# Performance work log

Hardware: AMD Instinct MI355X
Metric: run time of the kernel (lower is better)

Reference implementation:

```python
import jax, jax.numpy as jnp
import numpy as np

C_Z, H, C = 128, 4, 32
L = 320
SCALE = 1.0 / np.sqrt(C)
EPS = 1e-5


def setup_inputs() -> dict:
    key = jax.random.key(0)
    ks = jax.random.split(key, 8)
    s = 0.02
    return {
        "z": jax.random.normal(ks[0], (L, L, C_Z), dtype=jnp.float32),
        "pair_mask": jnp.ones((L, L), dtype=jnp.float32),
        "res_mask": jnp.ones((L,), dtype=bool),
        "ln_gamma": jnp.ones((C_Z,), dtype=jnp.float32),
        "ln_beta": jnp.zeros((C_Z,), dtype=jnp.float32),
        "Wq": jax.random.normal(ks[1], (C_Z, H * C), dtype=jnp.float32) * s,
        "Wk": jax.random.normal(ks[2], (C_Z, H * C), dtype=jnp.float32) * s,
        "Wv": jax.random.normal(ks[3], (C_Z, H * C), dtype=jnp.float32) * s,
        "Wb": jax.random.normal(ks[4], (C_Z, H), dtype=jnp.float32) * s,
        "Wg": jax.random.normal(ks[5], (C_Z, H * C), dtype=jnp.float32) * s,
        "Wout": jax.random.normal(ks[6], (H * C, C_Z), dtype=jnp.float32) * s,
    }


def _layernorm(x, gamma, beta):
    mu = jnp.mean(x, axis=-1, keepdims=True)
    var = jnp.mean(jnp.square(x - mu), axis=-1, keepdims=True)
    return (x - mu) * jax.lax.rsqrt(var + EPS) * gamma + beta


def reference(z, pair_mask, res_mask, ln_gamma, ln_beta, Wq, Wk, Wv, Wb, Wg, Wout):
    Ldim = z.shape[0]
    z_ln = _layernorm(z, ln_gamma, ln_beta)                      # [L,L,c_z]
    Q = (z_ln @ Wq).reshape(Ldim, Ldim, H, C)                    # [i,j,h,c]
    K = (z_ln @ Wk).reshape(Ldim, Ldim, H, C)                    # [i,k,h,c]
    V = (z_ln @ Wv).reshape(Ldim, Ldim, H, C)                    # [i,k,h,c]
    B = z_ln @ Wb                                                # [j,k,h]
    G = jax.nn.sigmoid(z_ln @ Wg).reshape(Ldim, Ldim, H, C)      # [i,j,h,c]

    # logits[i,h,j,k] = <Q[i,j], K[i,k]> * scale + B[j,k,h]
    logits = jnp.einsum("ijhc,ikhc->ihjk", Q, K) * SCALE
    logits = logits + jnp.transpose(B, (2, 0, 1))[None]          # +[1,h,j,k]
    neg_inf = jnp.asarray(-jnp.inf, logits.dtype)
    logits = jnp.where(res_mask[None, None, None, :], logits, neg_inf)
    attn = jax.nn.softmax(logits, axis=-1)                       # over k

    out = jnp.einsum("ihjk,ikhc->ijhc", attn, V)                 # [i,j,h,c]
    out = (G * out).reshape(Ldim, Ldim, H * C)
    dz = out @ Wout                                              # [L,L,c_z]
    return dz * pair_mask[..., None]
```

## Files before the change

### kernel.cpp

```cpp
#include <hip/hip_runtime.h>

#define LDIM 320
#define CZ 128
#define NH 4
#define CH 32
#define SCALE_QK 0.17677669529663687f
#define LN_EPS 1e-5f

typedef __attribute__((ext_vector_type(8))) short bf16x8;
typedef __attribute__((ext_vector_type(4))) float f32x4;

__device__ __forceinline__ unsigned int pack_bf2(float a, float b) {
  unsigned int ua = __float_as_uint(a);
  unsigned int ub = __float_as_uint(b);
  unsigned int ra = (ua + 0x7fffu + ((ua >> 16) & 1u)) >> 16;
  unsigned int rb = (ub + 0x7fffu + ((ub >> 16) & 1u)) >> 16;
  return (ra & 0xffffu) | (rb << 16);
}

__device__ __forceinline__ unsigned short f2bf(float a) {
  unsigned int ua = __float_as_uint(a);
  return (unsigned short)((ua + 0x7fffu + ((ua >> 16) & 1u)) >> 16);
}

__device__ __forceinline__ float bf2f(unsigned short u) {
  return __uint_as_float(((unsigned int)u) << 16);
}

__global__ __launch_bounds__(256) void k_prep(
    const float* __restrict__ Wq, const float* __restrict__ Wk,
    const float* __restrict__ Wv, const float* __restrict__ Wb,
    const float* __restrict__ Wg, const float* __restrict__ Wout,
    unsigned short* __restrict__ Wt, unsigned short* __restrict__ Woutt)
{
  __shared__ __attribute__((aligned(16))) unsigned short buf[64 * 136];
  const int t = threadIdx.x, bid = blockIdx.x;
  const bool isOut = (bid >= 9);
  const int n0 = isOut ? (bid - 9) * 64 : bid * 64;
  const int nl = t & 63;
  const int n = n0 + nl;
#pragma unroll 8
  for (int it = 0; it < 32; ++it) {
    const int k = (t >> 6) + 4 * it;
    float v;
    if (isOut)        v = Wout[k * 128 + n];
    else if (n < 128) v = Wq[k * 128 + n];
    else if (n < 256) v = Wk[k * 128 + n - 128];
    else if (n < 384) v = Wv[k * 128 + n - 256];
    else if (n < 512) v = Wg[k * 128 + n - 384];
    else if (n < 516) v = Wb[k * 4 + n - 512];
    else              v = 0.f;
    buf[nl * 136 + k] = f2bf(v);
  }
  __syncthreads();
  unsigned short* dst = isOut ? Woutt : Wt;
#pragma unroll
  for (int it = 0; it < 4; ++it) {
    const int idx = t + 256 * it;
    const int rr = idx >> 4, ck = idx & 15;
    const uint4 d = *(const uint4*)&buf[rr * 136 + ck * 8];
    *(uint4*)(dst + (size_t)(n0 + rr) * 128 + ck * 8) = d;
  }
}

__global__ __launch_bounds__(256) void k_lnproj(
    const float* __restrict__ z, const float* __restrict__ gamma,
    const float* __restrict__ beta, const unsigned short* __restrict__ Wt,
    unsigned short* __restrict__ Qg, unsigned short* __restrict__ Kg,
    unsigned short* __restrict__ Vg, unsigned short* __restrict__ Gg,
    float* __restrict__ Bh)
{
  __shared__ __attribute__((aligned(16))) unsigned short As[128 * 136];
  const int t = threadIdx.x;
  const int m0 = blockIdx.x * 128;
  const int rlane = t & 7;

  const float* gp = gamma + rlane * 16;
  const float* bp = beta + rlane * 16;
  const float4 g0 = *(const float4*)(gp + 0);
  const float4 g1 = *(const float4*)(gp + 4);
  const float4 g2 = *(const float4*)(gp + 8);
  const float4 g3 = *(const float4*)(gp + 12);
  const float4 b0 = *(const float4*)(bp + 0);
  const float4 b1 = *(const float4*)(bp + 4);
  const float4 b2 = *(const float4*)(bp + 8);
  const float4 b3 = *(const float4*)(bp + 12);

#pragma unroll
  for (int rr = 0; rr < 4; ++rr) {
    const int row = rr * 32 + (t >> 3);
    const float* zp = z + (size_t)(m0 + row) * CZ + rlane * 16;
    const float4 x0 = *(const float4*)(zp + 0);
    const float4 x1 = *(const float4*)(zp + 4);
    const float4 x2 = *(const float4*)(zp + 8);
    const float4 x3 = *(const float4*)(zp + 12);
    float s  = x0.x + x0.y + x0.z + x0.w + x1.x + x1.y + x1.z + x1.w +
               x2.x + x2.y + x2.z + x2.w + x3.x + x3.y + x3.z + x3.w;
    float ss = x0.x*x0.x + x0.y*x0.y + x0.z*x0.z + x0.w*x0.w +
               x1.x*x1.x + x1.y*x1.y + x1.z*x1.z + x1.w*x1.w +
               x2.x*x2.x + x2.y*x2.y + x2.z*x2.z + x2.w*x2.w +
               x3.x*x3.x + x3.y*x3.y + x3.z*x3.z + x3.w*x3.w;
    s  += __shfl_xor(s, 1);  ss += __shfl_xor(ss, 1);
    s  += __shfl_xor(s, 2);  ss += __shfl_xor(ss, 2);
    s  += __shfl_xor(s, 4);  ss += __shfl_xor(ss, 4);
    const float mu  = s * (1.f / 128.f);
    const float var = ss * (1.f / 128.f) - mu * mu;
    const float rs  = rsqrtf(var + LN_EPS);
    uint4 u0, u1;
    u0.x = pack_bf2((x0.x - mu) * rs * g0.x + b0.x, (x0.y - mu) * rs * g0.y + b0.y);
    u0.y = pack_bf2((x0.z - mu) * rs * g0.z + b0.z, (x0.w - mu) * rs * g0.w + b0.w);
    u0.z = pack_bf2((x1.x - mu) * rs * g1.x + b1.x, (x1.y - mu) * rs * g1.y + b1.y);
    u0.w = pack_bf2((x1.z - mu) * rs * g1.z + b1.z, (x1.w - mu) * rs * g1.w + b1.w);
    u1.x = pack_bf2((x2.x - mu) * rs * g2.x + b2.x, (x2.y - mu) * rs * g2.y + b2.y);
    u1.y = pack_bf2((x2.z - mu) * rs * g2.z + b2.z, (x2.w - mu) * rs * g2.w + b2.w);
    u1.z = pack_bf2((x3.x - mu) * rs * g3.x + b3.x, (x3.y - mu) * rs * g3.y + b3.y);
    u1.w = pack_bf2((x3.z - mu) * rs * g3.z + b3.z, (x3.w - mu) * rs * g3.w + b3.w);
    unsigned short* dst = &As[row * 136 + rlane * 16];
    *(uint4*)(dst + 0) = u0;
    *(uint4*)(dst + 8) = u1;
  }
  __syncthreads();

  const int w = t >> 6, lane = t & 63;
  const int m16 = lane & 15, qd = lane >> 4;
  const f32x4 z4 = {0.f, 0.f, 0.f, 0.f};

  bf16x8 af[2][4];
#pragma unroll
  for (int ks = 0; ks < 4; ++ks) {
    af[0][ks] = *(const bf16x8*)&As[(w * 32 + m16) * 136 + ks * 32 + qd * 8];
    af[1][ks] = *(const bf16x8*)&As[(w * 32 + 16 + m16) * 136 + ks * 32 + qd * 8];
  }

  for (int ntile = 0; ntile < 8; ++ntile) {
    f32x4 acc[2][4];
#pragma unroll
    for (int sub = 0; sub < 2; ++sub)
#pragma unroll
      for (int nt = 0; nt < 4; ++nt) acc[sub][nt] = z4;
#pragma unroll
    for (int ks = 0; ks < 4; ++ks) {
#pragma unroll
      for (int nt = 0; nt < 4; ++nt) {
        const bf16x8 bf = *(const bf16x8*)(
            Wt + (size_t)(ntile * 64 + nt * 16 + m16) * 128 + ks * 32 + qd * 8);
        acc[0][nt] = __builtin_amdgcn_mfma_f32_16x16x32_bf16(af[0][ks], bf, acc[0][nt], 0, 0, 0);
        acc[1][nt] = __builtin_amdgcn_mfma_f32_16x16x32_bf16(af[1][ks], bf, acc[1][nt], 0, 0, 0);
      }
    }
#pragma unroll
    for (int sub = 0; sub < 2; ++sub) {
#pragma unroll
      for (int r = 0; r < 4; ++r) {
        const int p = m0 + w * 32 + sub * 16 + qd * 4 + r;
        const int a = p / 320, bb = p - a * 320;
#pragma unroll
        for (int nt = 0; nt < 4; ++nt) {
          const int n = ntile * 64 + nt * 16 + m16;
          const int off = n & 127, hh = off >> 5, cc = off & 31;
          float val = acc[sub][nt][r];
          if (ntile >= 6) val = 1.f / (1.f + __expf(-val));
          unsigned short* dst =
              (ntile < 2 ? Qg : (ntile < 4 ? Kg : (ntile < 6 ? Vg : Gg)));
          dst[((size_t)(a * 4 + hh) * 320 + bb) * 32 + cc] = f2bf(val);
        }
      }
    }
  }

  {
    f32x4 acc0 = z4, acc1 = z4;
#pragma unroll
    for (int ks = 0; ks < 4; ++ks) {
      const bf16x8 bf = *(const bf16x8*)(
          Wt + (size_t)(512 + m16) * 128 + ks * 32 + qd * 8);
      acc0 = __builtin_amdgcn_mfma_f32_16x16x32_bf16(af[0][ks], bf, acc0, 0, 0, 0);
      acc1 = __builtin_amdgcn_mfma_f32_16x16x32_bf16(af[1][ks], bf, acc1, 0, 0, 0);
    }
    if (m16 < 4) {
#pragma unroll
      for (int r = 0; r < 4; ++r) {
        const int p0 = m0 + w * 32 + qd * 4 + r;
        Bh[(size_t)m16 * 102400 + p0] = acc0[r];
        Bh[(size_t)m16 * 102400 + p0 + 16] = acc1[r];
      }
    }
  }
}

__global__ __launch_bounds__(256) void k_attn(
    const unsigned short* __restrict__ Qg, const unsigned short* __restrict__ Kg,
    const unsigned short* __restrict__ Vg, const unsigned short* __restrict__ Gg,
    const float* __restrict__ Bh, const int* __restrict__ rmask,
    unsigned short* __restrict__ Obg)
{
  __shared__ __attribute__((aligned(16))) unsigned short Vt[32 * 328];
  __shared__ __attribute__((aligned(16))) unsigned short Ps[4][16 * 168];
  const int h = blockIdx.x, i = blockIdx.y;
  const int t = threadIdx.x;
  const size_t base = (size_t)(i * NH + h) * (LDIM * CH);

  {
    const int k0 = t >> 3, c4 = (t & 7) * 4;
#pragma unroll
    for (int it = 0; it < 10; ++it) {
      const int k = k0 + 32 * it;
      const uint2 d = *(const uint2*)(Vg + base + k * 32 + c4);
      Vt[(c4 + 0) * 328 + k] = (unsigned short)(d.x & 0xffffu);
      Vt[(c4 + 1) * 328 + k] = (unsigned short)(d.x >> 16);
      Vt[(c4 + 2) * 328 + k] = (unsigned short)(d.y & 0xffffu);
      Vt[(c4 + 3) * 328 + k] = (unsigned short)(d.y >> 16);
    }
  }
  __syncthreads();

  const int w = t >> 6, lane = t & 63;
  const int m16 = lane & 15, qd = lane >> 4;
  const f32x4 z4 = {0.f, 0.f, 0.f, 0.f};

  float mkr[20];
#pragma unroll
  for (int kt = 0; kt < 20; ++kt)
    mkr[kt] = rmask[kt * 16 + m16] ? 0.f : -INFINITY;

  for (int jt = w; jt < 20; jt += 4) {
    const bf16x8 qfrag =
        *(const bf16x8*)(Qg + base + (size_t)(jt * 16 + m16) * 32 + qd * 8);

    f32x4 acc[20];
#pragma unroll
    for (int kt = 0; kt < 20; ++kt) {
      const bf16x8 kf =
          *(const bf16x8*)(Kg + base + (size_t)(kt * 16 + m16) * 32 + qd * 8);
      acc[kt] = __builtin_amdgcn_mfma_f32_16x16x32_bf16(qfrag, kf, z4, 0, 0, 0);
    }

    const float* bp = Bh + (size_t)h * 102400 +
                      (size_t)(jt * 16 + qd * 4) * 320 + m16;
    float mx[4] = {-INFINITY, -INFINITY, -INFINITY, -INFINITY};
#pragma unroll
    for (int kt = 0; kt < 20; ++kt) {
#pragma unroll
      for (int r = 0; r < 4; ++r) {
        const float b = bp[r * 320 + kt * 16];
        const float s = fmaf(acc[kt][r], SCALE_QK, b) + mkr[kt];
        acc[kt][r] = s;
        mx[r] = fmaxf(mx[r], s);
      }
    }
#pragma unroll
    for (int r = 0; r < 4; ++r) {
      mx[r] = fmaxf(mx[r], __shfl_xor(mx[r], 1));
      mx[r] = fmaxf(mx[r], __shfl_xor(mx[r], 2));
      mx[r] = fmaxf(mx[r], __shfl_xor(mx[r], 4));
      mx[r] = fmaxf(mx[r], __shfl_xor(mx[r], 8));
    }
    float l[4] = {0.f, 0.f, 0.f, 0.f};
#pragma unroll
    for (int kt = 0; kt < 20; ++kt) {
#pragma unroll
      for (int r = 0; r < 4; ++r) {
        const float p = __expf(acc[kt][r] - mx[r]);
        acc[kt][r] = p;
        l[r] += p;
      }
    }
#pragma unroll
    for (int r = 0; r < 4; ++r) {
      l[r] += __shfl_xor(l[r], 1);
      l[r] += __shfl_xor(l[r], 2);
      l[r] += __shfl_xor(l[r], 4);
      l[r] += __shfl_xor(l[r], 8);
    }
    float rl[4];
#pragma unroll
    for (int r = 0; r < 4; ++r) rl[r] = 1.f / l[r];

    f32x4 accO0 = z4, accO1 = z4;
#pragma unroll
    for (int hh = 0; hh < 2; ++hh) {
      __syncthreads();
#pragma unroll
      for (int kt2 = 0; kt2 < 10; ++kt2) {
        const int kt = hh * 10 + kt2;
#pragma unroll
        for (int r = 0; r < 4; ++r)
          Ps[w][(qd * 4 + r) * 168 + kt2 * 16 + m16] = f2bf(acc[kt][r] * rl[r]);
      }
      __syncthreads();
#pragma unroll
      for (int ks = 0; ks < 5; ++ks) {
        const bf16x8 pf = *(const bf16x8*)&Ps[w][m16 * 168 + ks * 32 + qd * 8];
        const bf16x8 v0 =
            *(const bf16x8*)&Vt[m16 * 328 + hh * 160 + ks * 32 + qd * 8];
        const bf16x8 v1 =
            *(const bf16x8*)&Vt[(16 + m16) * 328 + hh * 160 + ks * 32 + qd * 8];
        accO0 = __builtin_amdgcn_mfma_f32_16x16x32_bf16(pf, v0, accO0, 0, 0, 0);
        accO1 = __builtin_amdgcn_mfma_f32_16x16x32_bf16(pf, v1, accO1, 0, 0, 0);
      }
    }

#pragma unroll
    for (int r = 0; r < 4; ++r) {
      const int j = jt * 16 + qd * 4 + r;
      const float g0 = bf2f(Gg[base + (size_t)j * 32 + m16]);
      const float g1 = bf2f(Gg[base + (size_t)j * 32 + 16 + m16]);
      unsigned short* op = Obg + (size_t)(i * 320 + j) * 128 + h * 32;
      op[m16]      = f2bf(g0 * accO0[r]);
      op[16 + m16] = f2bf(g1 * accO1[r]);
    }
  }
}

__global__ __launch_bounds__(256) void k_out(
    const unsigned short* __restrict__ Obg, const unsigned short* __restrict__ Woutt,
    const float* __restrict__ pm, float* __restrict__ out)
{
  __shared__ __attribute__((aligned(16))) unsigned short As[128 * 136];
  __shared__ __attribute__((aligned(16))) unsigned short Bs[64 * 136];
  const int t = threadIdx.x;
  const int ntile = blockIdx.x;
  const int m0 = blockIdx.y * 128;

#pragma unroll
  for (int it = 0; it < 8; ++it) {
    const int idx = t + 256 * it;
    const int rr = idx >> 4, ck = idx & 15;
    const uint4 d = *(const uint4*)(Obg + (size_t)(m0 + rr) * 128 + ck * 8);
    *(uint4*)&As[rr * 136 + ck * 8] = d;
  }
  {
    const unsigned short* wrow = Woutt + (size_t)ntile * 64 * 128;
#pragma unroll
    for (int it = 0; it < 4; ++it) {
      const int idx = t + 256 * it;
      const int n = idx >> 4, ck = idx & 15;
      const uint4 d = *(const uint4*)(wrow + n * 128 + ck * 8);
      *(uint4*)&Bs[n * 136 + ck * 8] = d;
    }
  }
  __syncthreads();

  const int w = t >> 6, lane = t & 63;
  const int m16 = lane & 15, qd = lane >> 4;
  const f32x4 z4 = {0.f, 0.f, 0.f, 0.f};
  f32x4 acc[2][4];
#pragma unroll
  for (int sub = 0; sub < 2; ++sub)
#pragma unroll
    for (int nt = 0; nt < 4; ++nt) acc[sub][nt] = z4;

#pragma unroll
  for (int ks = 0; ks < 4; ++ks) {
    const bf16x8 af0 = *(const bf16x8*)&As[(w * 32 + m16) * 136 + qd * 8 + ks * 32];
    const bf16x8 af1 = *(const bf16x8*)&As[(w * 32 + 16 + m16) * 136 + qd * 8 + ks * 32];
#pragma unroll
    for (int nt = 0; nt < 4; ++nt) {
      const bf16x8 bf = *(const bf16x8*)&Bs[(nt * 16 + m16) * 136 + qd * 8 + ks * 32];
      acc[0][nt] = __builtin_amdgcn_mfma_f32_16x16x32_bf16(af0, bf, acc[0][nt], 0, 0, 0);
      acc[1][nt] = __builtin_amdgcn_mfma_f32_16x16x32_bf16(af1, bf, acc[1][nt], 0, 0, 0);
    }
  }

#pragma unroll
  for (int sub = 0; sub < 2; ++sub) {
#pragma unroll
    for (int r = 0; r < 4; ++r) {
      const int p = m0 + w * 32 + sub * 16 + qd * 4 + r;
      const float m = pm[p];
      float* orow = out + (size_t)p * 128 + ntile * 64;
#pragma unroll
      for (int nt = 0; nt < 4; ++nt)
        orow[nt * 16 + m16] = acc[sub][nt][r] * m;
    }
  }
}

extern "C" void kernel_launch(void* const* d_in, const int* in_sizes, int n_in,
                              void* d_out, int out_size, void* d_ws, size_t ws_size,
                              hipStream_t stream)
{
  const float* z     = (const float*)d_in[0];
  const float* pmask = (const float*)d_in[1];
  const int*   rmask = (const int*)d_in[2];
  const float* gamma = (const float*)d_in[3];
  const float* beta  = (const float*)d_in[4];
  const float* Wq    = (const float*)d_in[5];
  const float* Wk    = (const float*)d_in[6];
  const float* Wv    = (const float*)d_in[7];
  const float* Wb    = (const float*)d_in[8];
  const float* Wg    = (const float*)d_in[9];
  const float* Wout  = (const float*)d_in[10];

  const size_t P = (size_t)LDIM * LDIM;
  const size_t E = P * 128;
  char* ws = (char*)d_ws;
  unsigned short* Qg = (unsigned short*)ws;
  unsigned short* Kg = Qg + E;
  unsigned short* Vg = Kg + E;
  unsigned short* Gg = Vg + E;
  unsigned short* Obg = Gg + E;
  unsigned short* Wt = Obg + E;
  unsigned short* Woutt = Wt + 576 * 128;
  float* Bh = (float*)(Woutt + 128 * 128);

  k_prep<<<dim3(11), 256, 0, stream>>>(Wq, Wk, Wv, Wb, Wg, Wout, Wt, Woutt);
  k_lnproj<<<dim3(800), 256, 0, stream>>>(z, gamma, beta, Wt,
                                          Qg, Kg, Vg, Gg, Bh);
  k_attn<<<dim3(NH, LDIM), 256, 0, stream>>>(Qg, Kg, Vg, Gg, Bh, rmask, Obg);
  k_out<<<dim3(2, 800), 256, 0, stream>>>(Obg, Woutt, pmask, (float*)d_out);
}
```

Before: 352.4 us.

## Emit transposed V from projection, fold scale into Wq and mask into bias

The projection kernel now writes V directly in a [a,h,c,k] transposed layout with packed stores. This lets the attention kernel read V fragments straight from global memory instead of staging a transpose in shared memory, and drops the block-wide barriers around the per-wave P buffer. The QK scale is folded into Wq during weight prep, and the residue mask is folded into the bias tensor, which removes per-element multiply and mask work in the softmax. The trade-off is uncoalesced global V reads per MFMA in place of LDS reads, plus 8-byte scattered writes in the projection.

```diff
diff --git a/kernel.cpp b/kernel.cpp
--- a/kernel.cpp
+++ b/kernel.cpp
@@ -44,7 +44,7 @@
     const int k = (t >> 6) + 4 * it;
     float v;
     if (isOut)        v = Wout[k * 128 + n];
-    else if (n < 128) v = Wq[k * 128 + n];
+    else if (n < 128) v = Wq[k * 128 + n] * SCALE_QK;
     else if (n < 256) v = Wk[k * 128 + n - 128];
     else if (n < 384) v = Wv[k * 128 + n - 256];
     else if (n < 512) v = Wg[k * 128 + n - 384];
@@ -66,8 +66,9 @@
 __global__ __launch_bounds__(256) void k_lnproj(
     const float* __restrict__ z, const float* __restrict__ gamma,
     const float* __restrict__ beta, const unsigned short* __restrict__ Wt,
+    const int* __restrict__ rmask,
     unsigned short* __restrict__ Qg, unsigned short* __restrict__ Kg,
-    unsigned short* __restrict__ Vg, unsigned short* __restrict__ Gg,
+    unsigned short* __restrict__ Vtg, unsigned short* __restrict__ Gg,
     float* __restrict__ Bh)
 {
   __shared__ __attribute__((aligned(16))) unsigned short As[128 * 136];
@@ -148,21 +149,37 @@
         acc[1][nt] = __builtin_amdgcn_mfma_f32_16x16x32_bf16(af[1][ks], bf, acc[1][nt], 0, 0, 0);
       }
     }
-#pragma unroll
-    for (int sub = 0; sub < 2; ++sub) {
-#pragma unroll
-      for (int r = 0; r < 4; ++r) {
-        const int p = m0 + w * 32 + sub * 16 + qd * 4 + r;
-        const int a = p / 320, bb = p - a * 320;
+    if (ntile == 4 || ntile == 5) {
+#pragma unroll
+      for (int sub = 0; sub < 2; ++sub) {
+        const int p0 = m0 + w * 32 + sub * 16 + qd * 4;
+        const int a = p0 / 320, bb = p0 - a * 320;
 #pragma unroll
         for (int nt = 0; nt < 4; ++nt) {
           const int n = ntile * 64 + nt * 16 + m16;
           const int off = n & 127, hh = off >> 5, cc = off & 31;
-          float val = acc[sub][nt][r];
-          if (ntile >= 6) val = 1.f / (1.f + __expf(-val));
-          unsigned short* dst =
-              (ntile < 2 ? Qg : (ntile < 4 ? Kg : (ntile < 6 ? Vg : Gg)));
-          dst[((size_t)(a * 4 + hh) * 320 + bb) * 32 + cc] = f2bf(val);
+          uint2 pk;
+          pk.x = pack_bf2(acc[sub][nt][0], acc[sub][nt][1]);
+          pk.y = pack_bf2(acc[sub][nt][2], acc[sub][nt][3]);
+          *(uint2*)(Vtg + (size_t)(a * 4 + hh) * 10240 + (size_t)cc * 320 + bb) = pk;
+        }
+      }
+    } else {
+#pragma unroll
+      for (int sub = 0; sub < 2; ++sub) {
+#pragma unroll
+        for (int r = 0; r < 4; ++r) {
+          const int p = m0 + w * 32 + sub * 16 + qd * 4 + r;
+          const int a = p / 320, bb = p - a * 320;
+#pragma unroll
+          for (int nt = 0; nt < 4; ++nt) {
+            const int n = ntile * 64 + nt * 16 + m16;
+            const int off = n & 127, hh = off >> 5, cc = off & 31;
+            float val = acc[sub][nt][r];
+            if (ntile >= 6) val = 1.f / (1.f + __expf(-val));
+            unsigned short* dst = (ntile < 2 ? Qg : (ntile < 4 ? Kg : Gg));
+            dst[((size_t)(a * 4 + hh) * 320 + bb) * 32 + cc] = f2bf(val);
+          }
         }
       }
     }
@@ -181,8 +198,11 @@
 #pragma unroll
       for (int r = 0; r < 4; ++r) {
         const int p0 = m0 + w * 32 + qd * 4 + r;
-        Bh[(size_t)m16 * 102400 + p0] = acc0[r];
-        Bh[(size_t)m16 * 102400 + p0 + 16] = acc1[r];
+        const int k0 = p0 % 320, k1 = (p0 + 16) % 320;
+        const float mk0 = rmask[k0] ? 0.f : -INFINITY;
+        const float mk1 = rmask[k1] ? 0.f : -INFINITY;
+        Bh[(size_t)m16 * 102400 + p0] = acc0[r] + mk0;
+        Bh[(size_t)m16 * 102400 + p0 + 16] = acc1[r] + mk1;
       }
     }
   }
@@ -190,38 +210,18 @@
 
 __global__ __launch_bounds__(256) void k_attn(
     const unsigned short* __restrict__ Qg, const unsigned short* __restrict__ Kg,
-    const unsigned short* __restrict__ Vg, const unsigned short* __restrict__ Gg,
-    const float* __restrict__ Bh, const int* __restrict__ rmask,
+    const unsigned short* __restrict__ Vtg, const unsigned short* __restrict__ Gg,
+    const float* __restrict__ Bh,
     unsigned short* __restrict__ Obg)
 {
-  __shared__ __attribute__((aligned(16))) unsigned short Vt[32 * 328];
   __shared__ __attribute__((aligned(16))) unsigned short Ps[4][16 * 168];
   const int h = blockIdx.x, i = blockIdx.y;
   const int t = threadIdx.x;
   const size_t base = (size_t)(i * NH + h) * (LDIM * CH);
 
-  {
-    const int k0 = t >> 3, c4 = (t & 7) * 4;
-#pragma unroll
-    for (int it = 0; it < 10; ++it) {
-      const int k = k0 + 32 * it;
-      const uint2 d = *(const uint2*)(Vg + base + k * 32 + c4);
-      Vt[(c4 + 0) * 328 + k] = (unsigned short)(d.x & 0xffffu);
-      Vt[(c4 + 1) * 328 + k] = (unsigned short)(d.x >> 16);
-      Vt[(c4 + 2) * 328 + k] = (unsigned short)(d.y & 0xffffu);
-      Vt[(c4 + 3) * 328 + k] = (unsigned short)(d.y >> 16);
-    }
-  }
-  __syncthreads();
-
   const int w = t >> 6, lane = t & 63;
   const int m16 = lane & 15, qd = lane >> 4;
   const f32x4 z4 = {0.f, 0.f, 0.f, 0.f};
-
-  float mkr[20];
-#pragma unroll
-  for (int kt = 0; kt < 20; ++kt)
-    mkr[kt] = rmask[kt * 16 + m16] ? 0.f : -INFINITY;
 
   for (int jt = w; jt < 20; jt += 4) {
     const bf16x8 qfrag =
@@ -242,8 +242,7 @@
     for (int kt = 0; kt < 20; ++kt) {
 #pragma unroll
       for (int r = 0; r < 4; ++r) {
-        const float b = bp[r * 320 + kt * 16];
-        const float s = fmaf(acc[kt][r], SCALE_QK, b) + mkr[kt];
+        const float s = acc[kt][r] + bp[r * 320 + kt * 16];
         acc[kt][r] = s;
         mx[r] = fmaxf(mx[r], s);
       }
@@ -279,7 +278,6 @@
     f32x4 accO0 = z4, accO1 = z4;
 #pragma unroll
     for (int hh = 0; hh < 2; ++hh) {
-      __syncthreads();
 #pragma unroll
       for (int kt2 = 0; kt2 < 10; ++kt2) {
         const int kt = hh * 10 + kt2;
@@ -287,14 +285,13 @@
         for (int r = 0; r < 4; ++r)
           Ps[w][(qd * 4 + r) * 168 + kt2 * 16 + m16] = f2bf(acc[kt][r] * rl[r]);
       }
-      __syncthreads();
 #pragma unroll
       for (int ks = 0; ks < 5; ++ks) {
         const bf16x8 pf = *(const bf16x8*)&Ps[w][m16 * 168 + ks * 32 + qd * 8];
-        const bf16x8 v0 =
-            *(const bf16x8*)&Vt[m16 * 328 + hh * 160 + ks * 32 + qd * 8];
-        const bf16x8 v1 =
-            *(const bf16x8*)&Vt[(16 + m16) * 328 + hh * 160 + ks * 32 + qd * 8];
+        const bf16x8 v0 = *(const bf16x8*)(
+            Vtg + base + (size_t)m16 * 320 + hh * 160 + ks * 32 + qd * 8);
+        const bf16x8 v1 = *(const bf16x8*)(
+            Vtg + base + (size_t)(16 + m16) * 320 + hh * 160 + ks * 32 + qd * 8);
         accO0 = __builtin_amdgcn_mfma_f32_16x16x32_bf16(pf, v0, accO0, 0, 0, 0);
         accO1 = __builtin_amdgcn_mfma_f32_16x16x32_bf16(pf, v1, accO1, 0, 0, 0);
       }
@@ -397,16 +394,16 @@
   char* ws = (char*)d_ws;
   unsigned short* Qg = (unsigned short*)ws;
   unsigned short* Kg = Qg + E;
-  unsigned short* Vg = Kg + E;
-  unsigned short* Gg = Vg + E;
+  unsigned short* Vtg = Kg + E;
+  unsigned short* Gg = Vtg + E;
   unsigned short* Obg = Gg + E;
   unsigned short* Wt = Obg + E;
   unsigned short* Woutt = Wt + 576 * 128;
   float* Bh = (float*)(Woutt + 128 * 128);
 
   k_prep<<<dim3(11), 256, 0, stream>>>(Wq, Wk, Wv, Wb, Wg, Wout, Wt, Woutt);
-  k_lnproj<<<dim3(800), 256, 0, stream>>>(z, gamma, beta, Wt,
-                                          Qg, Kg, Vg, Gg, Bh);
-  k_attn<<<dim3(NH, LDIM), 256, 0, stream>>>(Qg, Kg, Vg, Gg, Bh, rmask, Obg);
+  k_lnproj<<<dim3(800), 256, 0, stream>>>(z, gamma, beta, Wt, rmask,
+                                          Qg, Kg, Vtg, Gg, Bh);
+  k_attn<<<dim3(NH, LDIM), 256, 0, stream>>>(Qg, Kg, Vtg, Gg, Bh, Obg);
   k_out<<<dim3(2, 800), 256, 0, stream>>>(Obg, Woutt, pmask, (float*)d_out);
 }
```

Result: slower. 634.7 us (+80.1%).
